# Performance work log

Hardware: AMD Instinct MI355X
Metric: run time of the kernel (lower is better)

The kernel has to match this reference:

```python
import jax, jax.numpy as jnp
import numpy as np

BETA = 1.0  # commitment loss weight (beta=1.0 in VQKD.__init__)

def l2norm(x, eps=1e-12):
    return x / jnp.maximum(jnp.linalg.norm(x, axis=-1, keepdims=True), eps)

def setup_inputs() -> dict:
    key = jax.random.key(0)
    k0, k1, k2, k3 = jax.random.split(key, 4)
    B, N, D_ENC, D_CODE, K = 8, 4096, 768, 32, 8192
    std = 0.02  # trunc_normal_(std=0.02) init of task layers
    return {
        "features": jax.random.normal(k0, (B, N, D_ENC), jnp.float32),
        "enc_w1": jax.random.normal(k1, (D_ENC, D_ENC), jnp.float32) * std,
        "enc_b1": jnp.zeros((D_ENC,), jnp.float32),
        "enc_w2": jax.random.normal(k2, (D_ENC, D_CODE), jnp.float32) * std,
        "enc_b2": jnp.zeros((D_CODE,), jnp.float32),
        "codebook": jax.random.normal(k3, (K, D_CODE), jnp.float32),
    }

def reference(features, enc_w1, enc_b1, enc_w2, enc_b2, codebook):
    # encode_task_layer: Linear -> Tanh -> Linear (run in fp32, as in the autocast-disabled block)
    z = jnp.tanh(features @ enc_w1 + enc_b1) @ enc_w2 + enc_b2          # [B, N, C]
    # NormEMAVectorQuantizer: l2-normalize tokens and (EMA-normalized) codebook
    z = l2norm(z)
    emb = l2norm(codebook)                                              # [K, C]
    # squared euclidean distances  ||z||^2 - 2 z.e + ||e||^2  -> [B, N, K]
    d = (jnp.sum(z * z, axis=-1, keepdims=True)
         - 2.0 * jnp.einsum('bnc,kc->bnk', z, emb)
         + jnp.sum(emb * emb, axis=-1))
    idx = jnp.argmin(d, axis=-1)                                        # [B, N] int32
    z_q_raw = emb[idx]                                                  # gather [B, N, C]
    loss = BETA * jnp.mean((jax.lax.stop_gradient(z_q_raw) - z) ** 2)   # commitment loss
    z_q = z + jax.lax.stop_gradient(z_q_raw - z)                        # straight-through
    return z_q, loss, idx
```

## Files before the change

### kernel.cpp

```cpp
#include <hip/hip_runtime.h>
#include <hip/hip_bf16.h>
#include <cstdint>
#include <cstddef>


namespace {
constexpr int TOKENS = 8 * 4096;
constexpr int DENC   = 768;
constexpr int DC     = 32;
constexpr int KC     = 8192;
constexpr int BM = 128, BN = 128, BK = 32;
constexpr int NSTEP = DENC / BK;
constexpr float WSCALE = 1024.0f;
constexpr float HSCALE = 512.0f;
constexpr float SSCALE = 512.0f;
constexpr int SCH = 256;
}

typedef _Float16 f16x8 __attribute__((ext_vector_type(8)));
typedef float    f32x4 __attribute__((ext_vector_type(4)));

__device__ inline void split2(float v, _Float16& h, _Float16& l) {
  h = (_Float16)v;
  l = (_Float16)(v - (float)h);
}

__device__ inline void gload_lds16(const void* g, void* l) {
  __builtin_amdgcn_global_load_lds(
      (const __attribute__((address_space(1))) void*)g,
      (__attribute__((address_space(3))) void*)l, 16, 0, 0);
}

__global__ void ksplitW(const float* __restrict__ W1,
                        _Float16* __restrict__ Wh, _Float16* __restrict__ Wl) {
  int n = blockIdx.y;
  int k = blockIdx.x * 256 + threadIdx.x;
  float w = W1[(size_t)k * DENC + n] * WSCALE;
  _Float16 h, l; split2(w, h, l);
  Wh[(size_t)n * DENC + k] = h;
  Wl[(size_t)n * DENC + k] = l;
}

__global__ void ksplitW2(const float* __restrict__ W2,
                         _Float16* __restrict__ W2h, _Float16* __restrict__ W2l) {
  int i = blockIdx.x * 256 + threadIdx.x;
  int k = i >> 5, c = i & 31;
  float w = W2[(size_t)k * DC + c] * WSCALE;
  _Float16 h, l; split2(w, h, l);
  W2h[(size_t)c * DENC + k] = h;
  W2l[(size_t)c * DENC + k] = l;
}

__global__ void knorm_codes(const float* __restrict__ cb,
                            float* __restrict__ embn, float* __restrict__ se2,
                            _Float16* __restrict__ Eh, _Float16* __restrict__ El) {
  int t = blockIdx.x * blockDim.x + threadIdx.x;
  int k = t >> 5, c = t & 31;
  float v = cb[(size_t)k * DC + c];
  float ss = v * v;
  #pragma unroll
  for (int m = 16; m >= 1; m >>= 1) ss += __shfl_xor(ss, m, 32);
  float nrm = fmaxf(sqrtf(ss), 1e-12f);
  float vn = v / nrm;
  embn[(size_t)k * DC + c] = vn;
  _Float16 h, l; split2(vn * SSCALE, h, l);
  Eh[(size_t)k * DC + c] = h;
  El[(size_t)k * DC + c] = l;
  float s2 = vn * vn;
  #pragma unroll
  for (int m = 16; m >= 1; m >>= 1) s2 += __shfl_xor(s2, m, 32);
  if (c == 0) se2[k] = s2 * (SSCALE * SSCALE);
}

__global__ __launch_bounds__(256, 2)
void kgemm1(const float* __restrict__ X,
            const _Float16* __restrict__ Wh, const _Float16* __restrict__ Wl,
            const float* __restrict__ bias1, float* __restrict__ H) {
  __shared__ __align__(16) _Float16 Ah[2][4][BM][8], Al[2][4][BM][8];
  __shared__ __align__(16) _Float16 Bh[2][4][BN][8], Bl[2][4][BN][8];

  const int bid = blockIdx.x;
  const int xcd = bid & 7;
  const int w   = bid >> 3;
  const int n_t = w % 6;
  const int m_t = xcd * 32 + w / 6;
  const int m0 = m_t * BM, n0 = n_t * BN;

  const int t    = threadIdx.x;
  const int lane = t & 63;
  const int wv   = t >> 6;
  const int wm   = wv >> 1, wn = wv & 1;
  const int lrow = lane & 15;
  const int lgrp = lane >> 4;

  const int arow = t >> 1;
  const int ach  = t & 1;
  const float* xrow = X + (size_t)(m0 + arow) * DENC + ach * 16;

  const int bpl = wv >> 1, bch = wv & 1;
  const _Float16* wlane = (bpl ? Wl : Wh) + (size_t)(n0 + bch * 64 + lane) * DENC;

  f32x4 acc[4][4];
  #pragma unroll
  for (int i = 0; i < 4; ++i)
    #pragma unroll
    for (int j = 0; j < 4; ++j) acc[i][j] = (f32x4)0.0f;

  {
    float4 u0 = *(const float4*)(xrow + 0), u1 = *(const float4*)(xrow + 4);
    float4 u2 = *(const float4*)(xrow + 8), u3 = *(const float4*)(xrow + 12);
    float va[16] = {u0.x,u0.y,u0.z,u0.w, u1.x,u1.y,u1.z,u1.w,
                    u2.x,u2.y,u2.z,u2.w, u3.x,u3.y,u3.z,u3.w};
    #pragma unroll
    for (int j = 0; j < 2; ++j) {
      f16x8 hh, ll;
      #pragma unroll
      for (int e = 0; e < 8; ++e) { _Float16 h, l; split2(va[j*8+e], h, l); hh[e]=h; ll[e]=l; }
      *(f16x8*)&Ah[0][ach*2 + j][arow][0] = hh;
      *(f16x8*)&Al[0][ach*2 + j][arow][0] = ll;
    }
    _Float16 (*Bd)[4][BN][8] = bpl ? Bl : Bh;
    #pragma unroll
    for (int o = 0; o < 4; ++o)
      gload_lds16(wlane + o * 8, &Bd[0][o][bch*64 + lane][0]);
  }

  float4 pax[4];
  for (int s = 0; s < NSTEP; ++s) {
    const int cur = s & 1;
    __syncthreads();

    const bool more = (s + 1 < NSTEP);
    if (more) {
      const float* src = xrow + (s + 1) * BK;
      pax[0] = *(const float4*)(src + 0);  pax[1] = *(const float4*)(src + 4);
      pax[2] = *(const float4*)(src + 8);  pax[3] = *(const float4*)(src + 12);
      _Float16 (*Bd)[4][BN][8] = bpl ? Bl : Bh;
      const _Float16* wsrc = wlane + (s + 1) * BK;
      #pragma unroll
      for (int o = 0; o < 4; ++o)
        gload_lds16(wsrc + o * 8, &Bd[cur ^ 1][o][bch*64 + lane][0]);
    }

    f16x8 fah[4], fal[4], fbh[4], fbl[4];
    #pragma unroll
    for (int nf = 0; nf < 4; ++nf) {
      const int col = wn * 64 + nf * 16 + lrow;
      fbh[nf] = *(const f16x8*)&Bh[cur][lgrp][col][0];
      fbl[nf] = *(const f16x8*)&Bl[cur][lgrp][col][0];
    }
    #pragma unroll
    for (int mf = 0; mf < 4; ++mf) {
      const int row = wm * 64 + mf * 16 + lrow;
      fah[mf] = *(const f16x8*)&Ah[cur][lgrp][row][0];
      fal[mf] = *(const f16x8*)&Al[cur][lgrp][row][0];
    }
    #pragma unroll
    for (int mf = 0; mf < 4; ++mf)
      #pragma unroll
      for (int nf = 0; nf < 4; ++nf) {
        acc[mf][nf] = __builtin_amdgcn_mfma_f32_16x16x32_f16(fah[mf], fbh[nf], acc[mf][nf], 0, 0, 0);
        acc[mf][nf] = __builtin_amdgcn_mfma_f32_16x16x32_f16(fah[mf], fbl[nf], acc[mf][nf], 0, 0, 0);
        acc[mf][nf] = __builtin_amdgcn_mfma_f32_16x16x32_f16(fal[mf], fbh[nf], acc[mf][nf], 0, 0, 0);
      }

    if (more) {
      float va[16] = {pax[0].x,pax[0].y,pax[0].z,pax[0].w, pax[1].x,pax[1].y,pax[1].z,pax[1].w,
                      pax[2].x,pax[2].y,pax[2].z,pax[2].w, pax[3].x,pax[3].y,pax[3].z,pax[3].w};
      #pragma unroll
      for (int j = 0; j < 2; ++j) {
        f16x8 hh, ll;
        #pragma unroll
        for (int e = 0; e < 8; ++e) { _Float16 h, l; split2(va[j*8+e], h, l); hh[e]=h; ll[e]=l; }
        *(f16x8*)&Ah[cur ^ 1][ach*2 + j][arow][0] = hh;
        *(f16x8*)&Al[cur ^ 1][ach*2 + j][arow][0] = ll;
      }
    }
  }

  #pragma unroll
  for (int nf = 0; nf < 4; ++nf) {
    const int col = n0 + wn * 64 + nf * 16 + lrow;
    const float b = bias1[col];
    #pragma unroll
    for (int mf = 0; mf < 4; ++mf) {
      #pragma unroll
      for (int r = 0; r < 4; ++r) {
        const int row = m0 + wm * 64 + mf * 16 + lgrp * 4 + r;
        H[(size_t)row * DENC + col] = tanhf(acc[mf][nf][r] * (1.0f / WSCALE) + b);
      }
    }
  }
}

__global__ __launch_bounds__(128, 4)
void kgemm2(const float* __restrict__ H,
            const _Float16* __restrict__ W2h, const _Float16* __restrict__ W2l,
            const float* __restrict__ b2, float* __restrict__ zn) {
  const int t = threadIdx.x, lane = t & 63, wv = t >> 6;
  const int lrow = lane & 15, lgrp = lane >> 4;
  const int tb = blockIdx.x * 64 + wv * 32;

  const float* ap[2];
  #pragma unroll
  for (int mf = 0; mf < 2; ++mf)
    ap[mf] = H + (size_t)(tb + mf * 16 + lrow) * DENC + lgrp * 8;
  const _Float16* bh_p[2]; const _Float16* bl_p[2];
  #pragma unroll
  for (int nf = 0; nf < 2; ++nf) {
    size_t coff = (size_t)(nf * 16 + lrow) * DENC + lgrp * 8;
    bh_p[nf] = W2h + coff; bl_p[nf] = W2l + coff;
  }

  f32x4 acc[2][2];
  #pragma unroll
  for (int i = 0; i < 2; ++i)
    #pragma unroll
    for (int j = 0; j < 2; ++j) acc[i][j] = (f32x4)0.0f;

  for (int s = 0; s < DENC / 32; ++s) {
    const int koff = s * 32;
    f16x8 a_h[2], a_l[2], b_h[2], b_l[2];
    #pragma unroll
    for (int mf = 0; mf < 2; ++mf) {
      float4 u = *(const float4*)(ap[mf] + koff);
      float4 v = *(const float4*)(ap[mf] + koff + 4);
      float va[8] = {u.x,u.y,u.z,u.w, v.x,v.y,v.z,v.w};
      f16x8 hh, ll;
      #pragma unroll
      for (int e = 0; e < 8; ++e) { _Float16 h, l; split2(va[e] * HSCALE, h, l); hh[e]=h; ll[e]=l; }
      a_h[mf] = hh; a_l[mf] = ll;
    }
    #pragma unroll
    for (int nf = 0; nf < 2; ++nf) {
      b_h[nf] = *(const f16x8*)(bh_p[nf] + koff);
      b_l[nf] = *(const f16x8*)(bl_p[nf] + koff);
    }
    #pragma unroll
    for (int mf = 0; mf < 2; ++mf)
      #pragma unroll
      for (int nf = 0; nf < 2; ++nf) {
        acc[mf][nf] = __builtin_amdgcn_mfma_f32_16x16x32_f16(a_h[mf], b_h[nf], acc[mf][nf], 0, 0, 0);
        acc[mf][nf] = __builtin_amdgcn_mfma_f32_16x16x32_f16(a_h[mf], b_l[nf], acc[mf][nf], 0, 0, 0);
        acc[mf][nf] = __builtin_amdgcn_mfma_f32_16x16x32_f16(a_l[mf], b_h[nf], acc[mf][nf], 0, 0, 0);
      }
  }

  const float inv = 1.0f / (HSCALE * WSCALE);
  float bv[2];
  #pragma unroll
  for (int nf = 0; nf < 2; ++nf) bv[nf] = b2[nf * 16 + lrow];
  #pragma unroll
  for (int mf = 0; mf < 2; ++mf) {
    float z[2][4], ss[4];
    #pragma unroll
    for (int r = 0; r < 4; ++r) {
      #pragma unroll
      for (int nf = 0; nf < 2; ++nf) z[nf][r] = acc[mf][nf][r] * inv + bv[nf];
      float s2 = z[0][r] * z[0][r] + z[1][r] * z[1][r];
      #pragma unroll
      for (int m = 8; m >= 1; m >>= 1) s2 += __shfl_xor(s2, m, 16);
      ss[r] = s2;
    }
    #pragma unroll
    for (int r = 0; r < 4; ++r) {
      const int row = tb + mf * 16 + lgrp * 4 + r;
      float nrm = fmaxf(sqrtf(ss[r]), 1e-12f);
      #pragma unroll
      for (int nf = 0; nf < 2; ++nf)
        zn[(size_t)row * DC + nf * 16 + lrow] = z[nf][r] / nrm;
    }
  }
}

__device__ inline unsigned long long packkey(float d, int idx) {
  unsigned int u = __float_as_uint(d);
  u = (u & 0x80000000u) ? ~u : (u | 0x80000000u);
  return ((unsigned long long)u << 32) | (unsigned int)idx;
}

__global__ __launch_bounds__(256, 3)
void ksearch(const float* __restrict__ zn, const _Float16* __restrict__ Eh,
             const _Float16* __restrict__ El, const float* __restrict__ se2,
             unsigned long long* __restrict__ keys) {
  __shared__ __align__(16) _Float16 Bh[4][SCH][8], Bl[4][SCH][8];
  __shared__ float ce2[SCH];
  const int t = threadIdx.x, lane = t & 63, wv = t >> 6;
  const int tb  = blockIdx.x * 256 + wv * 64;
  const int cb0 = blockIdx.y * 1024;
  const int lr = lane & 15, ko = lane >> 4;

  f16x8 azh[4], azl[4];
  #pragma unroll
  for (int m = 0; m < 4; ++m) {
    const float* zp = zn + (size_t)(tb + m * 16 + lr) * DC + ko * 8;
    float4 u = *(const float4*)zp, v = *(const float4*)(zp + 4);
    float vals[8] = {u.x, u.y, u.z, u.w, v.x, v.y, v.z, v.w};
    f16x8 hh, ll;
    #pragma unroll
    for (int e = 0; e < 8; ++e) {
      _Float16 h, l; split2(vals[e] * SSCALE, h, l);
      hh[e] = h; ll[e] = l;
    }
    azh[m] = hh; azl[m] = ll;
  }

  float best[4][4]; int bi[4][4];
  #pragma unroll
  for (int m = 0; m < 4; ++m)
    #pragma unroll
    for (int r = 0; r < 4; ++r) { best[m][r] = 3.4e38f; bi[m][r] = 0; }

  f16x8 pb[8]; float pe2;

  for (int ch = 0; ch < 4; ++ch) {
    const int cb = cb0 + ch * SCH;
    #pragma unroll
    for (int it = 0; it < 8; ++it) {
      const _Float16* src = (it < 4) ? Eh : El;
      pb[it] = *(const f16x8*)&src[(size_t)(cb + t) * DC + (it & 3) * 8];
    }
    pe2 = se2[cb + t];
    __syncthreads();
    #pragma unroll
    for (int it = 0; it < 8; ++it) {
      _Float16 (*B)[SCH][8] = (it < 4) ? Bh : Bl;
      *(f16x8*)&B[it & 3][t][0] = pb[it];
    }
    ce2[t] = pe2;
    __syncthreads();

    #pragma unroll 4
    for (int f = 0; f < SCH / 16; ++f) {
      f16x8 bh = *(const f16x8*)&Bh[ko][f * 16 + lr][0];
      f16x8 bl = *(const f16x8*)&Bl[ko][f * 16 + lr][0];
      float e2v = ce2[f * 16 + lr];
      int  code = cb + f * 16 + lr;
      #pragma unroll
      for (int m = 0; m < 4; ++m) {
        f32x4 a = (f32x4)0.0f;
        a = __builtin_amdgcn_mfma_f32_16x16x32_f16(azh[m], bh, a, 0, 0, 0);
        a = __builtin_amdgcn_mfma_f32_16x16x32_f16(azh[m], bl, a, 0, 0, 0);
        a = __builtin_amdgcn_mfma_f32_16x16x32_f16(azl[m], bh, a, 0, 0, 0);
        #pragma unroll
        for (int r = 0; r < 4; ++r) {
          float d = fmaf(-2.0f, a[r], e2v);
          bool c = d < best[m][r];
          best[m][r] = c ? d : best[m][r];
          bi[m][r]   = c ? code : bi[m][r];
        }
      }
    }
  }

  #pragma unroll
  for (int m = 0; m < 4; ++m)
    #pragma unroll
    for (int r = 0; r < 4; ++r) {
      float bd = best[m][r]; int ix = bi[m][r];
      #pragma unroll
      for (int s = 1; s < 16; s <<= 1) {
        float od = __shfl_xor(bd, s);
        int   oi = __shfl_xor(ix, s);
        if (od < bd || (od == bd && oi < ix)) { bd = od; ix = oi; }
      }
      if ((lane & 15) == 0) {
        int token = tb + m * 16 + (lane >> 4) * 4 + r;
        atomicMin(&keys[token], packkey(bd, ix));
      }
    }
}

__global__ __launch_bounds__(1024)
void kfinal(const unsigned long long* __restrict__ keys,
            const float* __restrict__ zn, const float* __restrict__ embn,
            float* __restrict__ zq, float* __restrict__ loss,
            float* __restrict__ oidx) {
  __shared__ float red[32];
  int t = blockIdx.x * blockDim.x + threadIdx.x;
  int tok = t >> 5, c = t & 31;
  unsigned long long key = keys[tok];
  int idx = (int)(unsigned int)(key & 0xFFFFFFFFull);
  float q = embn[(size_t)idx * DC + c];
  float z = zn[t];
  zq[t] = z + (q - z);
  float d = q - z;
  float ss = d * d;
  #pragma unroll
  for (int m = 16; m >= 1; m >>= 1) ss += __shfl_xor(ss, m, 32);
  if (c == 0) {
    red[threadIdx.x >> 5] = ss;
    oidx[tok] = (float)idx;
  }
  __syncthreads();
  if (threadIdx.x < 32) {
    float v = red[threadIdx.x];
    #pragma unroll
    for (int m = 16; m >= 1; m >>= 1) v += __shfl_xor(v, m, 32);
    if (threadIdx.x == 0)
      atomicAdd(loss, v * (1.0f / (float)(TOKENS * DC)));
  }
}

extern "C" void kernel_launch(void* const* d_in, const int* in_sizes, int n_in,
                              void* d_out, int out_size, void* d_ws, size_t ws_size,
                              hipStream_t stream) {
  const float* X   = (const float*)d_in[0];
  const float* W1  = (const float*)d_in[1];
  const float* B1  = (const float*)d_in[2];
  const float* W2  = (const float*)d_in[3];
  const float* B2  = (const float*)d_in[4];
  const float* CB  = (const float*)d_in[5];

  float* out  = (float*)d_out;
  float* zq   = out;
  float* loss = out + (size_t)TOKENS * DC;
  float* oidx = loss + 1;

  char* ws = (char*)d_ws;
  size_t off = 0;
  float* H    = (float*)(ws + off); off += (size_t)TOKENS * DENC * 4;
  float* zn   = (float*)(ws + off); off += (size_t)TOKENS * DC * 4;
  float* embn = (float*)(ws + off); off += (size_t)KC * DC * 4;
  float* se2  = (float*)(ws + off); off += (size_t)KC * 4;
  _Float16* Eh = (_Float16*)(ws + off); off += (size_t)KC * DC * 2;
  _Float16* El = (_Float16*)(ws + off); off += (size_t)KC * DC * 2;
  unsigned long long* keys = (unsigned long long*)(ws + off);
  off += (size_t)TOKENS * 8;
  _Float16* W2h = (_Float16*)(ws + off); off += (size_t)DC * DENC * 2;
  _Float16* W2l = (_Float16*)(ws + off); off += (size_t)DC * DENC * 2;
  _Float16* W1h = (_Float16*)zn;
  _Float16* W1l = W1h + (size_t)DENC * DENC;

  hipMemsetAsync(loss, 0, sizeof(float), stream);
  hipMemsetAsync(keys, 0xFF, (size_t)TOKENS * 8, stream);

  ksplitW<<<dim3(DENC / 256, DENC), 256, 0, stream>>>(W1, W1h, W1l);
  ksplitW2<<<(DENC * DC) / 256, 256, 0, stream>>>(W2, W2h, W2l);
  knorm_codes<<<(KC * DC) / 256, 256, 0, stream>>>(CB, embn, se2, Eh, El);
  kgemm1<<<(TOKENS / BM) * (DENC / BN), 256, 0, stream>>>(X, W1h, W1l, B1, H);
  kgemm2<<<TOKENS / 64, 128, 0, stream>>>(H, W2h, W2l, B2, zn);
  ksearch<<<dim3(TOKENS / 256, KC / 1024), 256, 0, stream>>>(zn, Eh, El, se2, keys);
  kfinal<<<TOKENS * DC / 1024, 1024, 0, stream>>>(keys, zn, embn, zq, loss, oidx);
}
```

Baseline: 297.9 us.

## Load GEMM1 A fragments directly from global into registers, drop A LDS staging

```diff
diff --git a/kernel.cpp b/kernel.cpp
--- a/kernel.cpp
+++ b/kernel.cpp
@@ -72,12 +72,11 @@
   if (c == 0) se2[k] = s2 * (SSCALE * SSCALE);
 }
 
-__global__ __launch_bounds__(256, 2)
+__global__ __launch_bounds__(256, 3)
 void kgemm1(const float* __restrict__ X,
             const _Float16* __restrict__ Wh, const _Float16* __restrict__ Wl,
             const float* __restrict__ bias1, float* __restrict__ H) {
-  __shared__ __align__(16) _Float16 Ah[2][4][BM][8], Al[2][4][BM][8];
-  __shared__ __align__(16) _Float16 Bh[2][4][BN][8], Bl[2][4][BN][8];
+  __shared__ __align__(16) _Float16 Bs[2][2][4][BN][8];
 
   const int bid = blockIdx.x;
   const int xcd = bid & 7;
@@ -93,87 +92,72 @@
   const int lrow = lane & 15;
   const int lgrp = lane >> 4;
 
-  const int arow = t >> 1;
-  const int ach  = t & 1;
-  const float* xrow = X + (size_t)(m0 + arow) * DENC + ach * 16;
-
   const int bpl = wv >> 1, bch = wv & 1;
   const _Float16* wlane = (bpl ? Wl : Wh) + (size_t)(n0 + bch * 64 + lane) * DENC;
 
+  const float* xb[4];
+  #pragma unroll
+  for (int mf = 0; mf < 4; ++mf)
+    xb[mf] = X + (size_t)(m0 + wm * 64 + mf * 16 + lrow) * DENC + lgrp * 8;
+
   f32x4 acc[4][4];
   #pragma unroll
   for (int i = 0; i < 4; ++i)
     #pragma unroll
     for (int j = 0; j < 4; ++j) acc[i][j] = (f32x4)0.0f;
 
-  {
-    float4 u0 = *(const float4*)(xrow + 0), u1 = *(const float4*)(xrow + 4);
-    float4 u2 = *(const float4*)(xrow + 8), u3 = *(const float4*)(xrow + 12);
-    float va[16] = {u0.x,u0.y,u0.z,u0.w, u1.x,u1.y,u1.z,u1.w,
-                    u2.x,u2.y,u2.z,u2.w, u3.x,u3.y,u3.z,u3.w};
-    #pragma unroll
-    for (int j = 0; j < 2; ++j) {
-      f16x8 hh, ll;
-      #pragma unroll
-      for (int e = 0; e < 8; ++e) { _Float16 h, l; split2(va[j*8+e], h, l); hh[e]=h; ll[e]=l; }
-      *(f16x8*)&Ah[0][ach*2 + j][arow][0] = hh;
-      *(f16x8*)&Al[0][ach*2 + j][arow][0] = ll;
-    }
-    _Float16 (*Bd)[4][BN][8] = bpl ? Bl : Bh;
-    #pragma unroll
-    for (int o = 0; o < 4; ++o)
-      gload_lds16(wlane + o * 8, &Bd[0][o][bch*64 + lane][0]);
-  }
-
-  float4 pax[4];
+  float4 pax[8];
+  #pragma unroll
+  for (int o = 0; o < 4; ++o)
+    gload_lds16(wlane + o * 8, &Bs[0][bpl][o][bch * 64 + lane][0]);
+  #pragma unroll
+  for (int mf = 0; mf < 4; ++mf) {
+    pax[2 * mf]     = *(const float4*)(xb[mf]);
+    pax[2 * mf + 1] = *(const float4*)(xb[mf] + 4);
+  }
+
   for (int s = 0; s < NSTEP; ++s) {
     const int cur = s & 1;
     __syncthreads();
 
     const bool more = (s + 1 < NSTEP);
     if (more) {
-      const float* src = xrow + (s + 1) * BK;
-      pax[0] = *(const float4*)(src + 0);  pax[1] = *(const float4*)(src + 4);
-      pax[2] = *(const float4*)(src + 8);  pax[3] = *(const float4*)(src + 12);
-      _Float16 (*Bd)[4][BN][8] = bpl ? Bl : Bh;
       const _Float16* wsrc = wlane + (s + 1) * BK;
       #pragma unroll
       for (int o = 0; o < 4; ++o)
-        gload_lds16(wsrc + o * 8, &Bd[cur ^ 1][o][bch*64 + lane][0]);
-    }
-
-    f16x8 fah[4], fal[4], fbh[4], fbl[4];
+        gload_lds16(wsrc + o * 8, &Bs[cur ^ 1][bpl][o][bch * 64 + lane][0]);
+    }
+
+    f16x8 fah[4], fal[4];
+    #pragma unroll
+    for (int mf = 0; mf < 4; ++mf) {
+      float4 u = pax[2 * mf], v = pax[2 * mf + 1];
+      float va[8] = {u.x, u.y, u.z, u.w, v.x, v.y, v.z, v.w};
+      f16x8 hh, ll;
+      #pragma unroll
+      for (int e = 0; e < 8; ++e) { _Float16 h, l; split2(va[e], h, l); hh[e] = h; ll[e] = l; }
+      fah[mf] = hh; fal[mf] = ll;
+    }
+
+    if (more) {
+      #pragma unroll
+      for (int mf = 0; mf < 4; ++mf) {
+        const float* p = xb[mf] + (s + 1) * BK;
+        pax[2 * mf]     = *(const float4*)(p);
+        pax[2 * mf + 1] = *(const float4*)(p + 4);
+      }
+    }
+
     #pragma unroll
     for (int nf = 0; nf < 4; ++nf) {
       const int col = wn * 64 + nf * 16 + lrow;
-      fbh[nf] = *(const f16x8*)&Bh[cur][lgrp][col][0];
-      fbl[nf] = *(const f16x8*)&Bl[cur][lgrp][col][0];
-    }
-    #pragma unroll
-    for (int mf = 0; mf < 4; ++mf) {
-      const int row = wm * 64 + mf * 16 + lrow;
-      fah[mf] = *(const f16x8*)&Ah[cur][lgrp][row][0];
-      fal[mf] = *(const f16x8*)&Al[cur][lgrp][row][0];
-    }
-    #pragma unroll
-    for (int mf = 0; mf < 4; ++mf)
-      #pragma unroll
-      for (int nf = 0; nf < 4; ++nf) {
-        acc[mf][nf] = __builtin_amdgcn_mfma_f32_16x16x32_f16(fah[mf], fbh[nf], acc[mf][nf], 0, 0, 0);
-        acc[mf][nf] = __builtin_amdgcn_mfma_f32_16x16x32_f16(fah[mf], fbl[nf], acc[mf][nf], 0, 0, 0);
-        acc[mf][nf] = __builtin_amdgcn_mfma_f32_16x16x32_f16(fal[mf], fbh[nf], acc[mf][nf], 0, 0, 0);
-      }
-
-    if (more) {
-      float va[16] = {pax[0].x,pax[0].y,pax[0].z,pax[0].w, pax[1].x,pax[1].y,pax[1].z,pax[1].w,
-                      pax[2].x,pax[2].y,pax[2].z,pax[2].w, pax[3].x,pax[3].y,pax[3].z,pax[3].w};
-      #pragma unroll
-      for (int j = 0; j < 2; ++j) {
-        f16x8 hh, ll;
-        #pragma unroll
-        for (int e = 0; e < 8; ++e) { _Float16 h, l; split2(va[j*8+e], h, l); hh[e]=h; ll[e]=l; }
-        *(f16x8*)&Ah[cur ^ 1][ach*2 + j][arow][0] = hh;
-        *(f16x8*)&Al[cur ^ 1][ach*2 + j][arow][0] = ll;
+      f16x8 nbh = *(const f16x8*)&Bs[cur][0][lgrp][col][0];
+      f16x8 nbl = *(const f16x8*)&Bs[cur][1][lgrp][col][0];
+      #pragma unroll
+      for (int mf = 0; mf < 4; ++mf) {
+        acc[mf][nf] = __builtin_amdgcn_mfma_f32_16x16x32_f16(fah[mf], nbh, acc[mf][nf], 0, 0, 0);
+        acc[mf][nf] = __builtin_amdgcn_mfma_f32_16x16x32_f16(fah[mf], nbl, acc[mf][nf], 0, 0, 0);
+        acc[mf][nf] = __builtin_amdgcn_mfma_f32_16x16x32_f16(fal[mf], nbh, acc[mf][nf], 0, 0, 0);
       }
     }
   }
```

Measured after the change: 358.8 us. 1.2x slower.
